# Kernel optimization log

Measured on AMD Instinct MI355X. Metric: run time of the kernel, lower is better.

Reference implementation:

```python
import jax, jax.numpy as jnp
import numpy as np

N_NODES = 50000
N_EDGES = 800000
IN_CH = 128
HEADS = 4
OUT_CH = 32
NEG_SLOPE = 0.2


def setup_inputs() -> dict:
    key = jax.random.key(0)
    ks = jax.random.split(key, 8)
    x = jax.random.normal(ks[0], (N_NODES, IN_CH), dtype=jnp.float32)
    # edges guaranteed to have no self-loops (module removes then re-adds them)
    tgt = jax.random.randint(ks[1], (N_EDGES,), 0, N_NODES)
    off = jax.random.randint(ks[2], (N_EDGES,), 1, N_NODES)
    src = (tgt + off) % N_NODES
    edge_index = jnp.stack([src, tgt]).astype(jnp.int64)
    glorot = lambda k, shp: jax.random.uniform(
        k, shp, jnp.float32, -1.0, 1.0) * np.sqrt(6.0 / (shp[-1] + shp[-2]))
    Wl = glorot(ks[3], (HEADS * OUT_CH, IN_CH))  # torch Linear weight [out,in]
    Wr = glorot(ks[4], (HEADS * OUT_CH, IN_CH))
    att = glorot(ks[5], (1, HEADS, OUT_CH))
    bl = jnp.zeros((HEADS * OUT_CH,), jnp.float32)
    br = jnp.zeros((HEADS * OUT_CH,), jnp.float32)
    bias = jnp.zeros((HEADS * OUT_CH,), jnp.float32)
    return {"x": x, "edge_index": edge_index, "Wl": Wl, "bl": bl,
            "Wr": Wr, "br": br, "att": att, "bias": bias}


def _forward(x, edge_index, Wl, bl, Wr, br, att, bias):
    H, C = HEADS, OUT_CH
    n = x.shape[0]
    x_l = (x @ Wl.T + bl).reshape(n, H, C)  # target projection
    x_r = (x @ Wr.T + br).reshape(n, H, C)  # source projection
    # add self-loops (inputs contain none by construction)
    loops = jnp.arange(n, dtype=edge_index.dtype)
    src = jnp.concatenate([edge_index[0], loops])
    tgt = jnp.concatenate([edge_index[1], loops])
    x_i = x_l[tgt]                     # [E', H, C]
    x_j = x_r[src]                     # [E', H, C]
    a_in = jax.nn.leaky_relu(x_i + x_j, NEG_SLOPE)
    alpha = jnp.einsum('ehc,ohc->eh', a_in, att)  # [E', H]
    # segment softmax over target nodes
    m = jax.ops.segment_max(alpha, tgt, num_segments=n)
    alpha = jnp.exp(alpha - jax.lax.stop_gradient(m)[tgt])
    denom = jax.ops.segment_sum(alpha, tgt, num_segments=n)
    alpha = alpha / denom[tgt]
    msgs = x_j * alpha[:, :, None]     # [E', H, C]
    out = jax.ops.segment_sum(msgs, tgt, num_segments=n)  # [N, H, C]
    out = out.reshape(n, H * C) + bias  # concat=True
    return out


def reference(x, edge_index, Wl, bl, Wr, br, att, bias):
    return _forward(x, edge_index, Wl, bl, Wr, br, att, bias)
```

## Files before the change

kernel.cpp:

```cpp
#include <hip/hip_runtime.h>
#include <hip/hip_bf16.h>
#include <stdint.h>

#define N_NODES 50000
#define N_EDGES 800000
#define IN_CH   128
#define NEG_SLOPE 0.2f

#define NBUCK   98
#define E1      8000
#define FILLB   100
#define BCAP    12288
#define BSTRIDE 49152
#define CAPR    48

#define E_PER 8
#define FILL_BLOCKS 391

typedef short short8 __attribute__((ext_vector_type(8)));
typedef float f32x4  __attribute__((ext_vector_type(4)));
typedef float f32x2  __attribute__((ext_vector_type(2)));

static __device__ __forceinline__ float bf_lo(uint32_t p) { return __uint_as_float(p << 16); }
static __device__ __forceinline__ float bf_hi(uint32_t p) { return __uint_as_float(p & 0xffff0000u); }
static __device__ __forceinline__ uint16_t f_to_bf(float f) {
    uint32_t u = __float_as_uint(f);
    u += 0x7fffu + ((u >> 16) & 1u);
    return (uint16_t)(u >> 16);
}

static __device__ __forceinline__ f32x2 lrelu2(f32x2 x) {
    f32x2 s = x * NEG_SLOPE;
    f32x2 r;
    r[0] = fmaxf(x[0], s[0]);
    r[1] = fmaxf(x[1], s[1]);
    return r;
}

static __device__ __forceinline__ float sum16(float x) {
    x += __uint_as_float(__builtin_amdgcn_update_dpp(0, __float_as_uint(x), 0xB1,  0xf, 0xf, true));
    x += __uint_as_float(__builtin_amdgcn_update_dpp(0, __float_as_uint(x), 0x4E,  0xf, 0xf, true));
    x += __uint_as_float(__builtin_amdgcn_update_dpp(0, __float_as_uint(x), 0x141, 0xf, 0xf, true));
    x += __uint_as_float(__builtin_amdgcn_update_dpp(0, __float_as_uint(x), 0x140, 0xf, 0xf, true));
    return x;
}

static __device__ __forceinline__ void sum16x2(float& a, float& b) {
    asm("s_nop 0\n\t"
        "v_add_f32 %0, %0, %0 quad_perm:[1,0,3,2] row_mask:0xf bank_mask:0xf bound_ctrl:0\n\t"
        "v_add_f32 %1, %1, %1 quad_perm:[1,0,3,2] row_mask:0xf bank_mask:0xf bound_ctrl:0\n\t"
        "v_add_f32 %0, %0, %0 quad_perm:[2,3,0,1] row_mask:0xf bank_mask:0xf bound_ctrl:0\n\t"
        "v_add_f32 %1, %1, %1 quad_perm:[2,3,0,1] row_mask:0xf bank_mask:0xf bound_ctrl:0\n\t"
        "v_add_f32 %0, %0, %0 row_half_mirror row_mask:0xf bank_mask:0xf bound_ctrl:0\n\t"
        "v_add_f32 %1, %1, %1 row_half_mirror row_mask:0xf bank_mask:0xf bound_ctrl:0\n\t"
        "v_add_f32 %0, %0, %0 row_mirror row_mask:0xf bank_mask:0xf bound_ctrl:0\n\t"
        "v_add_f32 %1, %1, %1 row_mirror row_mask:0xf bank_mask:0xf bound_ctrl:0"
        : "+v"(a), "+v"(b));
}

static __device__ __forceinline__ void wswz_body(
    int t, const float* __restrict__ Wl, const float* __restrict__ Wr,
    __hip_bfloat16* __restrict__ wswz)
{
    int ct = t >> 8, rem = t & 255;
    int ch = rem >> 6, lane = rem & 63;
    int m = lane & 15, quad = lane >> 4;
    const float* W = (ct < 8) ? Wl : Wr;
    int o = ((ct & 7) << 4) + m;
    const float* src = W + (size_t)o * IN_CH + ch * 32 + quad * 8;
    short8 f;
#pragma unroll
    for (int j = 0; j < 8; ++j) f[j] = (short)f_to_bf(src[j]);
    *(short8*)((short*)wswz + (size_t)t * 8) = f;
}

static __device__ __forceinline__ void proj_body(
    int rowbase, int tid,
    const float* __restrict__ x, const __hip_bfloat16* __restrict__ wswz,
    const float* __restrict__ bl, const float* __restrict__ br,
    float* __restrict__ xl, __hip_bfloat16* __restrict__ xr)
{
    int lane = tid & 63;
    int widx = tid >> 6;
    int m = lane & 15;
    int quad = lane >> 4;

    short8 afrag[4];
    const float* xrow = x + (size_t)(rowbase + m) * IN_CH;
#pragma unroll
    for (int ch = 0; ch < 4; ++ch) {
        f32x4 p0 = *(const f32x4*)(xrow + ch * 32 + quad * 8);
        f32x4 p1 = *(const f32x4*)(xrow + ch * 32 + quad * 8 + 4);
        short8 f;
#pragma unroll
        for (int j = 0; j < 4; ++j) { f[j] = (short)f_to_bf(p0[j]); f[j + 4] = (short)f_to_bf(p1[j]); }
        afrag[ch] = f;
    }

    const short* wz = (const short*)wswz;
    const float* bv = (widx < 2) ? bl : br;
#pragma unroll
    for (int cc = 0; cc < 4; ++cc) {
        int ct = widx * 4 + cc;
        int o = ((ct & 7) << 4) + m;
        f32x4 acc = {0.f, 0.f, 0.f, 0.f};
#pragma unroll
        for (int ch = 0; ch < 4; ++ch) {
            short8 bfrag = *(const short8*)(wz + ((size_t)(ct * 4 + ch) * 64 + lane) * 8);
            acc = __builtin_amdgcn_mfma_f32_16x16x32_bf16(afrag[ch], bfrag, acc, 0, 0, 0);
        }
        float bias_v = bv[o];
        if (widx < 2) {
#pragma unroll
            for (int r = 0; r < 4; ++r)
                xl[(size_t)(rowbase + quad * 4 + r) * IN_CH + o] = acc[r] + bias_v;
        } else {
#pragma unroll
            for (int r = 0; r < 4; ++r)
                xr[(size_t)(rowbase + quad * 4 + r) * IN_CH + o] = __float2bfloat16(acc[r] + bias_v);
        }
    }
}

__global__ __launch_bounds__(256) void prep_kernel(
    const float* __restrict__ Wl, const float* __restrict__ Wr,
    __hip_bfloat16* __restrict__ wswz, int* __restrict__ z, int zn)
{
    int t = blockIdx.x * 256 + threadIdx.x;
    if (t < 4096) wswz_body(t, Wl, Wr, wswz);
    for (int i = t; i < zn; i += 64 * 256) z[i] = 0;
}

__global__ __launch_bounds__(256) void proj_fill(
    const float* __restrict__ x, const __hip_bfloat16* __restrict__ wswz,
    const float* __restrict__ bl, const float* __restrict__ br,
    float* __restrict__ xl, __hip_bfloat16* __restrict__ xr,
    const int* __restrict__ ei, uint32_t* __restrict__ bcnt,
    char* __restrict__ region)
{
    __shared__ uint32_t s_sorted[E1];
    __shared__ uint32_t s_hist[NBUCK], s_lstart[NBUCK], s_loc[NBUCK], s_gbase[NBUCK];
    __shared__ uint32_t s_T;

    if (blockIdx.x >= FILLB) {
        proj_body((blockIdx.x - FILLB) * 16, threadIdx.x, x, wswz, bl, br, xl, xr);
        return;
    }

    int tid = threadIdx.x;
    int fb = blockIdx.x;
    for (int i = tid; i < NBUCK; i += 256) s_hist[i] = 0;
    __syncthreads();

    const uint32_t* eiw = (const uint32_t*)ei;
    bool zlo = (eiw[2 * (tid & 63) + 1] == 0u);
    bool is64 = __popcll(__ballot(zlo)) >= 32;
    int e0 = fb * E1;

    for (int k = tid; k < E1; k += 256) {
        int e = e0 + k;
        int s = is64 ? (int)eiw[2 * (size_t)e] : ei[e];
        int t = is64 ? (int)eiw[2 * ((size_t)N_EDGES + e)] : ei[N_EDGES + e];
        if ((unsigned)s < N_NODES && (unsigned)t < N_NODES)
            atomicAdd(&s_hist[t >> 9], 1u);
    }
    __syncthreads();

    if (tid < NBUCK) s_gbase[tid] = atomicAdd(&bcnt[tid], s_hist[tid]);
    if (tid == 0) {
        uint32_t acc = 0;
        for (int i = 0; i < NBUCK; ++i) { s_lstart[i] = acc; acc += s_hist[i]; }
        s_T = acc;
    }
    __syncthreads();
    if (tid < NBUCK) s_loc[tid] = s_lstart[tid];
    __syncthreads();

    for (int k = tid; k < E1; k += 256) {
        int e = e0 + k;
        int s = is64 ? (int)eiw[2 * (size_t)e] : ei[e];
        int t = is64 ? (int)eiw[2 * ((size_t)N_EDGES + e)] : ei[N_EDGES + e];
        if ((unsigned)s < N_NODES && (unsigned)t < N_NODES) {
            uint32_t r = atomicAdd(&s_loc[t >> 9], 1u);
            s_sorted[r] = ((uint32_t)t << 16) | (uint32_t)s;
        }
    }
    __syncthreads();

    int T = (int)s_T;
    for (int k = tid; k < T; k += 256) {
        uint32_t v = s_sorted[k];
        uint32_t key = v >> 25;
        uint32_t g = s_gbase[key] + (uint32_t)k - s_lstart[key];
        if (g < BCAP)
            ((uint32_t*)(region + (size_t)key * BSTRIDE))[g] = v;
    }
}

__global__ __launch_bounds__(256) void csr_build(
    const uint32_t* __restrict__ bcnt, char* __restrict__ region,
    uint32_t* __restrict__ degs32)
{
    __shared__ uint16_t slab[512 * CAPR];
    __shared__ uint32_t lcnt[512];
    int b = blockIdx.x, tid = threadIdx.x;
    for (int i = tid; i < 512; i += 256) lcnt[i] = 0;
    __syncthreads();

    uint32_t* reg = (uint32_t*)(region + (size_t)b * BSTRIDE);
    int M = min((int)bcnt[b], BCAP);
    for (int k = tid; k < M; k += 256) {
        uint32_t v = reg[k];
        int node = (int)((v >> 16) & 511u);
        uint32_t pos = atomicAdd(&lcnt[node], 1u);
        if (pos < CAPR) slab[node * CAPR + pos] = (uint16_t)(v & 0xffffu);
    }
    __syncthreads();

    const uint32_t* sw = (const uint32_t*)slab;
    for (int j = tid; j < (512 * CAPR / 2); j += 256) reg[j] = sw[j];
    if (tid < 128) {
        uint32_t p = 0;
#pragma unroll
        for (int q = 0; q < 4; ++q) {
            uint32_t d = min(lcnt[tid * 4 + q], (uint32_t)CAPR);
            p |= d << (q * 8);
        }
        degs32[b * 128 + tid] = p;
    }
}

__global__ __launch_bounds__(256) void fill_kernel(
    const int* __restrict__ ei, int cap,
    int* __restrict__ cnt, uint16_t* __restrict__ csr)
{
    const uint32_t* eiw = (const uint32_t*)ei;
    bool z = (eiw[2 * (threadIdx.x & 63) + 1] == 0u);
    bool is64 = __popcll(__ballot(z)) >= 32;

    int tid = blockIdx.x * 256 + threadIdx.x;
    int e0 = tid * E_PER;
    if (e0 >= N_EDGES) return;

    int src[E_PER], tgt[E_PER];
    if (is64) {
        const int4* ps = (const int4*)(eiw + 2 * (size_t)e0);
        const int4* pt = (const int4*)(eiw + 2 * ((size_t)N_EDGES + e0));
#pragma unroll
        for (int k = 0; k < 4; ++k) {
            int4 s = ps[k], t = pt[k];
            src[2 * k] = s.x; src[2 * k + 1] = s.z;
            tgt[2 * k] = t.x; tgt[2 * k + 1] = t.z;
        }
    } else {
        const int4* ps = (const int4*)(ei + e0);
        const int4* pt = (const int4*)(ei + N_EDGES + e0);
#pragma unroll
        for (int k = 0; k < 2; ++k) {
            int4 s = ps[k], t = pt[k];
            src[4 * k] = s.x; src[4 * k + 1] = s.y; src[4 * k + 2] = s.z; src[4 * k + 3] = s.w;
            tgt[4 * k] = t.x; tgt[4 * k + 1] = t.y; tgt[4 * k + 2] = t.z; tgt[4 * k + 3] = t.w;
        }
    }

    int pos[E_PER];
#pragma unroll
    for (int k = 0; k < E_PER; ++k) {
        bool ok = (unsigned)src[k] < N_NODES && (unsigned)tgt[k] < N_NODES;
        pos[k] = ok ? atomicAdd(&cnt[tgt[k]], 1) : cap;
    }
#pragma unroll
    for (int k = 0; k < E_PER; ++k)
        if (pos[k] < cap) csr[(size_t)tgt[k] * cap + pos[k]] = (uint16_t)src[k];
}

__global__ __launch_bounds__(256) void proj_kernel(
    const float* __restrict__ x, const __hip_bfloat16* __restrict__ wswz,
    const float* __restrict__ bl, const float* __restrict__ br,
    float* __restrict__ xl, __hip_bfloat16* __restrict__ xr)
{
    proj_body(blockIdx.x * 16, threadIdx.x, x, wswz, bl, br, xl, xr);
}

__global__ __launch_bounds__(256) void agg_kernel(
    const __hip_bfloat16* __restrict__ xr,
    const char* __restrict__ degbase, int degpacked,
    const uint16_t* __restrict__ csr, int ldcsr, int cap,
    const float* __restrict__ att, const float* __restrict__ bias,
    float* out )
{
    int n = blockIdx.x * 4 + (threadIdx.x >> 6);
    if (n >= N_NODES) return;
    int lane = threadIdx.x & 63;

    const uint32_t* xrw = (const uint32_t*)xr;

    f32x2 qv = *(const f32x2*)(out + (size_t)n * IN_CH + 2 * lane);
    f32x2 av = *(const f32x2*)(att + 2 * lane);
    f32x2 bv = *(const f32x2*)(bias + 2 * lane);

    int deg;
    if (degpacked) {
        uint32_t pk = ((const uint32_t*)degbase)[n >> 2];
        deg = (int)((pk >> ((n & 3) * 8)) & 255u);
    } else {
        deg = ((const int*)degbase)[n];
    }
    deg = min(deg, cap);

    const uint16_t* lst = csr + (size_t)n * ldcsr;
    int idxreg = (int)lst[min(lane, cap - 1)];

    uint32_t u = xrw[(size_t)n * 64 + lane];
    f32x2 a0v; a0v[0] = bf_lo(u); a0v[1] = bf_hi(u);
    f32x2 p0 = lrelu2(qv + a0v) * av;
    float t = sum16(p0[0] + p0[1]);
    float w = __expf(t);
    float lsum = w;
    f32x2 acc = w * a0v;

    if (deg > 0) {
        int dm1 = deg - 1;
        int s0a = __builtin_amdgcn_readlane(idxreg, 0);
        int s0b = __builtin_amdgcn_readlane(idxreg, min(1, dm1));
        int s1a = __builtin_amdgcn_readlane(idxreg, min(2, dm1));
        int s1b = __builtin_amdgcn_readlane(idxreg, min(3, dm1));
        uint32_t uA0 = xrw[(size_t)s0a * 64 + lane];
        uint32_t uB0 = xrw[(size_t)s0b * 64 + lane];
        uint32_t uA1 = xrw[(size_t)s1a * 64 + lane];
        uint32_t uB1 = xrw[(size_t)s1b * 64 + lane];
        int i = 0;
        while (i + 1 < deg) {
            int s2a = __builtin_amdgcn_readlane(idxreg, min(i + 4, dm1));
            int s2b = __builtin_amdgcn_readlane(idxreg, min(i + 5, dm1));
            uint32_t uA2 = xrw[(size_t)s2a * 64 + lane];
            uint32_t uB2 = xrw[(size_t)s2b * 64 + lane];

            f32x2 aA; aA[0] = bf_lo(uA0); aA[1] = bf_hi(uA0);
            f32x2 aB; aB[0] = bf_lo(uB0); aB[1] = bf_hi(uB0);
            f32x2 pA = lrelu2(qv + aA) * av;
            f32x2 pB = lrelu2(qv + aB) * av;
            float tA = pA[0] + pA[1];
            float tB = pB[0] + pB[1];
            sum16x2(tA, tB);
            float wA = __expf(tA), wB = __expf(tB);
            lsum += wA + wB;
            acc += wA * aA;
            acc += wB * aB;

            uA0 = uA1; uB0 = uB1;
            uA1 = uA2; uB1 = uB2;
            i += 2;
        }
        if (i < deg) {
            f32x2 aA; aA[0] = bf_lo(uA0); aA[1] = bf_hi(uA0);
            f32x2 pA = lrelu2(qv + aA) * av;
            float tA = sum16(pA[0] + pA[1]);
            float wA = __expf(tA);
            lsum += wA;
            acc += wA * aA;
        }
    }

    float inv = 1.f / lsum;
    f32x2 ov = acc * inv + bv;
    *(f32x2*)(out + (size_t)n * IN_CH + 2 * lane) = ov;
}

extern "C" void kernel_launch(void* const* d_in, const int* in_sizes, int n_in,
                              void* d_out, int out_size, void* d_ws, size_t ws_size,
                              hipStream_t stream) {
    const float* x    = (const float*)d_in[0];
    const int*   ei   = (const int*)d_in[1];
    const float* Wl   = (const float*)d_in[2];
    const float* bl   = (const float*)d_in[3];
    const float* Wr   = (const float*)d_in[4];
    const float* br   = (const float*)d_in[5];
    const float* att  = (const float*)d_in[6];
    const float* bias = (const float*)d_in[7];
    float* out = (float*)d_out;

    char* ws = (char*)d_ws;
    __hip_bfloat16* xr   = (__hip_bfloat16*)(ws);
    __hip_bfloat16* wswz = (__hip_bfloat16*)(ws + 12800000);

    const size_t DEGS_OFF = 12865536;
    const size_t BCNT_OFF = 12915712;
    const size_t REG_OFF  = 12916224;
    const size_t NEED     = REG_OFF + (size_t)NBUCK * BSTRIDE;

    if (ws_size >= NEED) {
        uint32_t* degs   = (uint32_t*)(ws + DEGS_OFF);
        uint32_t* bcnt   = (uint32_t*)(ws + BCNT_OFF);
        char*     region = ws + REG_OFF;

        prep_kernel<<<64, 256, 0, stream>>>(Wl, Wr, wswz, (int*)bcnt, 128);
        proj_fill<<<FILLB + N_NODES / 16, 256, 0, stream>>>(
            x, wswz, bl, br, out, xr, ei, bcnt, region);
        csr_build<<<NBUCK, 256, 0, stream>>>(bcnt, region, degs);
        agg_kernel<<<N_NODES / 4, 256, 0, stream>>>(
            xr, (const char*)degs, 1, (const uint16_t*)region, CAPR, CAPR,
            att, bias, out);
    } else {
        const size_t CSR_BASE = 13065536;
        int*      cnt = (int*)(ws + 12865536);
        uint16_t* csr = (uint16_t*)(ws + CSR_BASE);
        long long avail = (ws_size > CSR_BASE) ? (long long)(ws_size - CSR_BASE) : 0;
        int cap = (int)(avail / ((long long)N_NODES * 2));
        if (cap > 64) cap = 64;
        if (cap < 1)  cap = 1;

        prep_kernel<<<64, 256, 0, stream>>>(Wl, Wr, wswz, cnt, N_NODES);
        fill_kernel<<<FILL_BLOCKS, 256, 0, stream>>>(ei, cap, cnt, csr);
        proj_kernel<<<N_NODES / 16, 256, 0, stream>>>(x, wswz, bl, br, out, xr);
        agg_kernel<<<N_NODES / 4, 256, 0, stream>>>(
            xr, (const char*)cnt, 0, csr, cap, cap, att, bias, out);
    }
}
```

Measured before the change: 177.5 us.

## Halve bucket size for CSR build, deepen gather prefetch, use exp2

```diff
diff --git a/kernel.cpp b/kernel.cpp
--- a/kernel.cpp
+++ b/kernel.cpp
@@ -7,11 +7,11 @@
 #define IN_CH   128
 #define NEG_SLOPE 0.2f
 
-#define NBUCK   98
-#define E1      8000
-#define FILLB   100
-#define BCAP    12288
-#define BSTRIDE 49152
+#define NBUCK   196
+#define E1      4000
+#define FILLB   200
+#define BCAP    6144
+#define BSTRIDE 24576
 #define CAPR    48
 
 #define E_PER 8
@@ -162,7 +162,7 @@
         int s = is64 ? (int)eiw[2 * (size_t)e] : ei[e];
         int t = is64 ? (int)eiw[2 * ((size_t)N_EDGES + e)] : ei[N_EDGES + e];
         if ((unsigned)s < N_NODES && (unsigned)t < N_NODES)
-            atomicAdd(&s_hist[t >> 9], 1u);
+            atomicAdd(&s_hist[t >> 8], 1u);
     }
     __syncthreads();
 
@@ -181,7 +181,7 @@
         int s = is64 ? (int)eiw[2 * (size_t)e] : ei[e];
         int t = is64 ? (int)eiw[2 * ((size_t)N_EDGES + e)] : ei[N_EDGES + e];
         if ((unsigned)s < N_NODES && (unsigned)t < N_NODES) {
-            uint32_t r = atomicAdd(&s_loc[t >> 9], 1u);
+            uint32_t r = atomicAdd(&s_loc[t >> 8], 1u);
             s_sorted[r] = ((uint32_t)t << 16) | (uint32_t)s;
         }
     }
@@ -190,7 +190,7 @@
     int T = (int)s_T;
     for (int k = tid; k < T; k += 256) {
         uint32_t v = s_sorted[k];
-        uint32_t key = v >> 25;
+        uint32_t key = v >> 24;
         uint32_t g = s_gbase[key] + (uint32_t)k - s_lstart[key];
         if (g < BCAP)
             ((uint32_t*)(region + (size_t)key * BSTRIDE))[g] = v;
@@ -201,32 +201,32 @@
     const uint32_t* __restrict__ bcnt, char* __restrict__ region,
     uint32_t* __restrict__ degs32)
 {
-    __shared__ uint16_t slab[512 * CAPR];
-    __shared__ uint32_t lcnt[512];
+    __shared__ uint16_t slab[256 * CAPR];
+    __shared__ uint32_t lcnt[256];
     int b = blockIdx.x, tid = threadIdx.x;
-    for (int i = tid; i < 512; i += 256) lcnt[i] = 0;
+    lcnt[tid] = 0;
     __syncthreads();
 
     uint32_t* reg = (uint32_t*)(region + (size_t)b * BSTRIDE);
     int M = min((int)bcnt[b], BCAP);
     for (int k = tid; k < M; k += 256) {
         uint32_t v = reg[k];
-        int node = (int)((v >> 16) & 511u);
+        int node = (int)((v >> 16) & 255u);
         uint32_t pos = atomicAdd(&lcnt[node], 1u);
         if (pos < CAPR) slab[node * CAPR + pos] = (uint16_t)(v & 0xffffu);
     }
     __syncthreads();
 
     const uint32_t* sw = (const uint32_t*)slab;
-    for (int j = tid; j < (512 * CAPR / 2); j += 256) reg[j] = sw[j];
-    if (tid < 128) {
+    for (int j = tid; j < (256 * CAPR / 2); j += 256) reg[j] = sw[j];
+    if (tid < 64) {
         uint32_t p = 0;
 #pragma unroll
         for (int q = 0; q < 4; ++q) {
             uint32_t d = min(lcnt[tid * 4 + q], (uint32_t)CAPR);
             p |= d << (q * 8);
         }
-        degs32[b * 128 + tid] = p;
+        degs32[b * 64 + tid] = p;
     }
 }
 
@@ -297,6 +297,7 @@
 
     f32x2 qv = *(const f32x2*)(out + (size_t)n * IN_CH + 2 * lane);
     f32x2 av = *(const f32x2*)(att + 2 * lane);
+    av = av * 1.44269504088896f;
     f32x2 bv = *(const f32x2*)(bias + 2 * lane);
 
     int deg;
@@ -315,26 +316,30 @@
     f32x2 a0v; a0v[0] = bf_lo(u); a0v[1] = bf_hi(u);
     f32x2 p0 = lrelu2(qv + a0v) * av;
     float t = sum16(p0[0] + p0[1]);
-    float w = __expf(t);
+    float w = __builtin_amdgcn_exp2f(t);
     float lsum = w;
     f32x2 acc = w * a0v;
 
     if (deg > 0) {
         int dm1 = deg - 1;
-        int s0a = __builtin_amdgcn_readlane(idxreg, 0);
-        int s0b = __builtin_amdgcn_readlane(idxreg, min(1, dm1));
-        int s1a = __builtin_amdgcn_readlane(idxreg, min(2, dm1));
-        int s1b = __builtin_amdgcn_readlane(idxreg, min(3, dm1));
-        uint32_t uA0 = xrw[(size_t)s0a * 64 + lane];
-        uint32_t uB0 = xrw[(size_t)s0b * 64 + lane];
-        uint32_t uA1 = xrw[(size_t)s1a * 64 + lane];
-        uint32_t uB1 = xrw[(size_t)s1b * 64 + lane];
+        int sA0 = __builtin_amdgcn_readlane(idxreg, 0);
+        int sB0 = __builtin_amdgcn_readlane(idxreg, min(1, dm1));
+        int sA1 = __builtin_amdgcn_readlane(idxreg, min(2, dm1));
+        int sB1 = __builtin_amdgcn_readlane(idxreg, min(3, dm1));
+        int sA2 = __builtin_amdgcn_readlane(idxreg, min(4, dm1));
+        int sB2 = __builtin_amdgcn_readlane(idxreg, min(5, dm1));
+        uint32_t uA0 = xrw[(size_t)sA0 * 64 + lane];
+        uint32_t uB0 = xrw[(size_t)sB0 * 64 + lane];
+        uint32_t uA1 = xrw[(size_t)sA1 * 64 + lane];
+        uint32_t uB1 = xrw[(size_t)sB1 * 64 + lane];
+        uint32_t uA2 = xrw[(size_t)sA2 * 64 + lane];
+        uint32_t uB2 = xrw[(size_t)sB2 * 64 + lane];
         int i = 0;
         while (i + 1 < deg) {
-            int s2a = __builtin_amdgcn_readlane(idxreg, min(i + 4, dm1));
-            int s2b = __builtin_amdgcn_readlane(idxreg, min(i + 5, dm1));
-            uint32_t uA2 = xrw[(size_t)s2a * 64 + lane];
-            uint32_t uB2 = xrw[(size_t)s2b * 64 + lane];
+            int sA3 = __builtin_amdgcn_readlane(idxreg, min(i + 6, dm1));
+            int sB3 = __builtin_amdgcn_readlane(idxreg, min(i + 7, dm1));
+            uint32_t uA3 = xrw[(size_t)sA3 * 64 + lane];
+            uint32_t uB3 = xrw[(size_t)sB3 * 64 + lane];
 
             f32x2 aA; aA[0] = bf_lo(uA0); aA[1] = bf_hi(uA0);
             f32x2 aB; aB[0] = bf_lo(uB0); aB[1] = bf_hi(uB0);
@@ -343,20 +348,21 @@
             float tA = pA[0] + pA[1];
             float tB = pB[0] + pB[1];
             sum16x2(tA, tB);
-            float wA = __expf(tA), wB = __expf(tB);
+            float wA = __builtin_amdgcn_exp2f(tA), wB = __builtin_amdgcn_exp2f(tB);
             lsum += wA + wB;
             acc += wA * aA;
             acc += wB * aB;
 
             uA0 = uA1; uB0 = uB1;
             uA1 = uA2; uB1 = uB2;
+            uA2 = uA3; uB2 = uB3;
             i += 2;
         }
         if (i < deg) {
             f32x2 aA; aA[0] = bf_lo(uA0); aA[1] = bf_hi(uA0);
             f32x2 pA = lrelu2(qv + aA) * av;
             float tA = sum16(pA[0] + pA[1]);
-            float wA = __expf(tA);
+            float wA = __builtin_amdgcn_exp2f(tA);
             lsum += wA;
             acc += wA * aA;
         }
@@ -386,7 +392,7 @@
 
     const size_t DEGS_OFF = 12865536;
     const size_t BCNT_OFF = 12915712;
-    const size_t REG_OFF  = 12916224;
+    const size_t REG_OFF  = 12916736;
     const size_t NEED     = REG_OFF + (size_t)NBUCK * BSTRIDE;
 
     if (ws_size >= NEED) {
@@ -394,7 +400,7 @@
         uint32_t* bcnt   = (uint32_t*)(ws + BCNT_OFF);
         char*     region = ws + REG_OFF;
 
-        prep_kernel<<<64, 256, 0, stream>>>(Wl, Wr, wswz, (int*)bcnt, 128);
+        prep_kernel<<<64, 256, 0, stream>>>(Wl, Wr, wswz, (int*)bcnt, NBUCK);
         proj_fill<<<FILLB + N_NODES / 16, 256, 0, stream>>>(
             x, wswz, bl, br, out, xr, ei, bcnt, region);
         csr_build<<<NBUCK, 256, 0, stream>>>(bcnt, region, degs);
```

After: 164.5 us. -7.3%, faster.
